# Performance work log

Measured on AMD Instinct MI355X. Metric: run time of the kernel, lower is better.

The kernel has to match this reference:

```python
import jax, jax.numpy as jnp
import numpy as np


def setup_inputs() -> dict:
    key = jax.random.key(0)
    ks = jax.random.split(key, 8)
    B, N, H = 8, 64, 256
    nE, E = 256, 64
    HID, OUT = 512, 1
    s1 = 1.0 / np.sqrt(H + E)
    s2 = 1.0 / np.sqrt(HID)
    return {
        "h_all": jax.random.normal(ks[0], (B, N, H), dtype=jnp.float32),
        "e_feat": jax.random.normal(ks[1], (nE, E), dtype=jnp.float32),
        "W1": jax.random.normal(ks[2], (H + E, HID), dtype=jnp.float32) * s1,
        "b1": jnp.zeros((HID,), dtype=jnp.float32),
        "W2": jax.random.normal(ks[3], (HID, HID), dtype=jnp.float32) * s2,
        "b2": jnp.zeros((HID,), dtype=jnp.float32),
        "W3": jax.random.normal(ks[4], (HID, OUT), dtype=jnp.float32) * s2,
        "b3": jnp.zeros((OUT,), dtype=jnp.float32),
    }


def reference(h_all, e_feat, W1, b1, W2, b2, W3, b3):
    # Math == MLP(cat([expand(h), expand(e)], -1)) but computed via split
    # weights: cat([h,e]) @ W1 == h @ W1[:H] + e @ W1[H:], avoiding the
    # materialized [B,N,nE,H+E] concat tensor.
    H = h_all.shape[-1]
    Wh, We = W1[:H], W1[H:]
    h_part = jnp.einsum("bnh,hk->bnk", h_all, Wh)        # [B,N,HID]
    e_part = jnp.einsum("ed,dk->ek", e_feat, We)          # [nE,HID]
    x = h_part[:, :, None, :] + e_part[None, None, :, :] + b1  # [B,N,nE,HID]
    x = jax.nn.relu(x)
    x = jax.nn.relu(jnp.einsum("bnek,kj->bnej", x, W2) + b2)
    return jnp.einsum("bnek,ko->bneo", x, W3) + b3        # [B,N,nE,OUT]
```

## Files before the change

kernel.cpp:

```cpp
#include <hip/hip_runtime.h>
#include <hip/hip_bf16.h>


typedef __attribute__((ext_vector_type(8))) short bf16x8;
typedef __attribute__((ext_vector_type(4))) float f32x4;

static __device__ __forceinline__ ushort2 pk_bf16(float a, float b) {
  union { __hip_bfloat162 h; ushort2 u; } c;
  c.h = __float22bfloat162_rn(make_float2(a, b));
  return c.u;
}
static __device__ __forceinline__ float bf2f(unsigned short u) {
  union { unsigned int i; float f; } c;
  c.i = ((unsigned int)u) << 16;
  return c.f;
}

__global__ __launch_bounds__(256) void k_prep(
    const float* __restrict__ h_all, const float* __restrict__ e_feat,
    const float* __restrict__ W1, const float* __restrict__ b1,
    const float* __restrict__ W2,
    unsigned short* __restrict__ hpb, unsigned short* __restrict__ epb,
    unsigned short* __restrict__ w2f) {
  __shared__ float sm[64 * 68];
  const int t = threadIdx.x;
  const int b = blockIdx.x;

  if (b < 256) {
    const int r0 = b * 2;
    float (*hs)[256] = (float(*)[256])sm;
    hs[0][t] = h_all[(size_t)r0 * 256 + t];
    hs[1][t] = h_all[(size_t)(r0 + 1) * 256 + t];
    __syncthreads();
    float2 a0 = make_float2(0.f, 0.f), a1 = make_float2(0.f, 0.f);
    #pragma unroll 2
    for (int k = 0; k < 256; k += 4) {
      float2 w0 = *(const float2*)(W1 + (size_t)k * 512 + 2 * t);
      float2 w1 = *(const float2*)(W1 + (size_t)(k + 1) * 512 + 2 * t);
      float2 w2v = *(const float2*)(W1 + (size_t)(k + 2) * 512 + 2 * t);
      float2 w3v = *(const float2*)(W1 + (size_t)(k + 3) * 512 + 2 * t);
      float h00 = hs[0][k], h01 = hs[0][k + 1], h02 = hs[0][k + 2], h03 = hs[0][k + 3];
      float h10 = hs[1][k], h11 = hs[1][k + 1], h12 = hs[1][k + 2], h13 = hs[1][k + 3];
      a0.x = fmaf(h00, w0.x, a0.x); a0.y = fmaf(h00, w0.y, a0.y);
      a1.x = fmaf(h10, w0.x, a1.x); a1.y = fmaf(h10, w0.y, a1.y);
      a0.x = fmaf(h01, w1.x, a0.x); a0.y = fmaf(h01, w1.y, a0.y);
      a1.x = fmaf(h11, w1.x, a1.x); a1.y = fmaf(h11, w1.y, a1.y);
      a0.x = fmaf(h02, w2v.x, a0.x); a0.y = fmaf(h02, w2v.y, a0.y);
      a1.x = fmaf(h12, w2v.x, a1.x); a1.y = fmaf(h12, w2v.y, a1.y);
      a0.x = fmaf(h03, w3v.x, a0.x); a0.y = fmaf(h03, w3v.y, a0.y);
      a1.x = fmaf(h13, w3v.x, a1.x); a1.y = fmaf(h13, w3v.y, a1.y);
    }
    float2 bv = *(const float2*)(b1 + 2 * t);
    *(ushort2*)(hpb + (size_t)r0 * 512 + 2 * t) = pk_bf16(a0.x + bv.x, a0.y + bv.y);
    *(ushort2*)(hpb + (size_t)(r0 + 1) * 512 + 2 * t) = pk_bf16(a1.x + bv.x, a1.y + bv.y);
  } else if (b < 288) {
    const int r0 = (b - 256) * 8;
    sm[t] = e_feat[(size_t)r0 * 64 + t];
    sm[256 + t] = e_feat[(size_t)r0 * 64 + 256 + t];
    __syncthreads();
    float2 acc[8];
    #pragma unroll
    for (int i = 0; i < 8; ++i) acc[i] = make_float2(0.f, 0.f);
    for (int k = 0; k < 64; ++k) {
      float2 wv = *(const float2*)(W1 + (size_t)(256 + k) * 512 + 2 * t);
      #pragma unroll
      for (int i = 0; i < 8; ++i) {
        acc[i].x = fmaf(sm[i * 64 + k], wv.x, acc[i].x);
        acc[i].y = fmaf(sm[i * 64 + k], wv.y, acc[i].y);
      }
    }
    #pragma unroll
    for (int i = 0; i < 8; ++i)
      *(ushort2*)(epb + (size_t)(r0 + i) * 512 + 2 * t) = pk_bf16(acc[i].x, acc[i].y);
  } else {
    const int bb = b - 288;
    const int k0 = (bb >> 3) * 64;
    const int c0 = (bb & 7) * 64;
    #pragma unroll
    for (int rr = 0; rr < 4; ++rr) {
      const int row = rr * 16 + (t >> 4);
      float4 v = *(const float4*)(W2 + (size_t)(k0 + row) * 512 + c0 + (t & 15) * 4);
      *(float4*)(&sm[row * 68 + (t & 15) * 4]) = v;
    }
    __syncthreads();
    #pragma unroll
    for (int s2 = 0; s2 < 2; ++s2) {
      const int s = t * 2 + s2;
      const int rec = s >> 6, l = s & 63;
      const int jg = (c0 >> 4) + (rec & 3);
      const int ksg = (k0 >> 5) + (rec >> 2);
      const int cl = (rec & 3) * 16 + (l & 15);
      const int kl = (rec >> 2) * 32 + (l >> 4) * 8;
      union { ushort2 o[4]; uint4 v; } u;
      #pragma unroll
      for (int uu = 0; uu < 4; ++uu)
        u.o[uu] = pk_bf16(sm[(kl + 2 * uu) * 68 + cl], sm[(kl + 2 * uu + 1) * 68 + cl]);
      *(uint4*)(w2f + ((size_t)(jg * 16 + ksg) * 64 + l) * 8) = u.v;
    }
  }
}

__global__ __launch_bounds__(256, 2) void k_main(
    const unsigned short* __restrict__ hpb, const unsigned short* __restrict__ epb,
    const unsigned short* __restrict__ w2f, const float* __restrict__ b2,
    const float* __restrict__ W3, const float* __restrict__ b3,
    float* __restrict__ out) {
  __shared__ unsigned short x1s[64 * 512];

  const int t = threadIdx.x;
  const int lane = t & 63;
  const int w = t >> 6;
  const int l15 = lane & 15, l4 = lane >> 4;
  const int bn = blockIdx.x >> 2;
  const int e0 = (blockIdx.x & 3) << 6;
  const int off = (blockIdx.x * 11) & 15;
  const unsigned short* hprow = hpb + (size_t)bn * 512;

  const unsigned short* wrec = w2f + (size_t)w * 65536 + (size_t)lane * 8;
  bf16x8 bb[2][8];
  #pragma unroll
  for (int j = 0; j < 8; ++j) {
    bb[0][j] = *(const bf16x8*)(wrec + j * 8192 + (size_t)off * 512);
    bb[1][j] = *(const bf16x8*)(wrec + j * 8192 + (size_t)((off + 1) & 15) * 512);
  }

  {
    const int kk = t & 63;
    const int rbase = t >> 6;
    union { uint4 v; unsigned short s[8]; } hv, ev, ov;
    hv.v = *(const uint4*)(hprow + kk * 8);
    float hf[8];
    #pragma unroll
    for (int u = 0; u < 8; ++u) hf[u] = bf2f(hv.s[u]);
    #pragma unroll 2
    for (int rr = 0; rr < 16; ++rr) {
      const int r = rr * 4 + rbase;
      ev.v = *(const uint4*)(epb + (size_t)(e0 + r) * 512 + kk * 8);
      #pragma unroll
      for (int u = 0; u < 4; ++u) {
        ushort2 p = pk_bf16(fmaxf(bf2f(ev.s[2 * u]) + hf[2 * u], 0.f),
                            fmaxf(bf2f(ev.s[2 * u + 1]) + hf[2 * u + 1], 0.f));
        ov.s[2 * u] = p.x;
        ov.s[2 * u + 1] = p.y;
      }
      *(uint4*)(&x1s[r * 512 + (kk ^ (r & 7)) * 8]) = ov.v;
    }
  }
  __syncthreads();

  f32x4 acc[4][8] = {};
  #pragma unroll 4
  for (int ks = 0; ks < 16; ++ks) {
    const int cur = ks & 1;
    const int kr = (ks + off) & 15;
    const int kr2 = (ks + 2 + off) & 15;
    bf16x8 a[4];
    #pragma unroll
    for (int i = 0; i < 4; ++i) {
      const int r = i * 16 + l15;
      a[i] = *(const bf16x8*)(&x1s[r * 512 + (((kr * 4 + l4) ^ (l15 & 7)) * 8)]);
    }
    #pragma unroll
    for (int i = 0; i < 4; ++i)
      #pragma unroll
      for (int j = 0; j < 8; ++j)
        acc[i][j] = __builtin_amdgcn_mfma_f32_16x16x32_bf16(a[i], bb[cur][j], acc[i][j], 0, 0, 0);
    #pragma unroll
    for (int j = 0; j < 8; ++j)
      bb[cur][j] = *(const bf16x8*)(wrec + j * 8192 + (size_t)kr2 * 512);
  }

  float part[16];
  #pragma unroll
  for (int u = 0; u < 16; ++u) part[u] = 0.f;
  #pragma unroll
  for (int j = 0; j < 8; ++j) {
    const int n = w * 128 + j * 16 + l15;
    const float b2v = b2[n], w3v = W3[n];
    #pragma unroll
    for (int i = 0; i < 4; ++i)
      #pragma unroll
      for (int r = 0; r < 4; ++r)
        part[i * 4 + r] = fmaf(fmaxf(acc[i][j][r] + b2v, 0.f), w3v, part[i * 4 + r]);
  }
  #pragma unroll
  for (int u = 0; u < 16; ++u) {
    float v = part[u];
    v += __shfl_xor(v, 1);
    v += __shfl_xor(v, 2);
    v += __shfl_xor(v, 4);
    v += __shfl_xor(v, 8);
    part[u] = v;
  }
  __syncthreads();
  float* osum = (float*)x1s;
  if (l15 == 0) {
    #pragma unroll
    for (int i = 0; i < 4; ++i)
      #pragma unroll
      for (int r = 0; r < 4; ++r)
        osum[w * 64 + i * 16 + l4 * 4 + r] = part[i * 4 + r];
  }
  __syncthreads();
  if (t < 64) {
    float s = b3[0] + osum[t] + osum[64 + t] + osum[128 + t] + osum[192 + t];
    out[(size_t)bn * 256 + e0 + t] = s;
  }
}

extern "C" void kernel_launch(void* const* d_in, const int* in_sizes, int n_in,
                              void* d_out, int out_size, void* d_ws, size_t ws_size,
                              hipStream_t stream) {
  const float* h_all  = (const float*)d_in[0];
  const float* e_feat = (const float*)d_in[1];
  const float* W1     = (const float*)d_in[2];
  const float* b1     = (const float*)d_in[3];
  const float* W2     = (const float*)d_in[4];
  const float* b2     = (const float*)d_in[5];
  const float* W3     = (const float*)d_in[6];
  const float* b3     = (const float*)d_in[7];
  float* out = (float*)d_out;

  unsigned short* hpb = (unsigned short*)d_ws;
  unsigned short* epb = hpb + 512 * 512;
  unsigned short* w2f = epb + 256 * 512;

  hipLaunchKernelGGL(k_prep, dim3(352), dim3(256), 0, stream,
                     h_all, e_feat, W1, b1, W2, hpb, epb, w2f);
  hipLaunchKernelGGL(k_main, dim3(2048), dim3(256), 0, stream,
                     hpb, epb, w2f, b2, W3, b3, out);
}
```

Before: 145.1 us.

## Persistent k_main with register-resident W2 slice and double-buffered x1 tiles

k_main becomes a persistent kernel: 512 blocks of 512 threads, each keeping its half of the W2 columns (a 32-column strip per wave) resident in registers for the whole run. It loops over 8 tiles, building the next relu(h+e) tile in a second LDS buffer while MFMAs consume the current one, so W2 is no longer reloaded from global memory for every tile. Splitting the hidden dimension in two adds a partial-sum workspace and a third combine kernel that adds the halves and b3. This costs higher register pressure (32 bf16x8 fragments per lane), more LDS, and an extra launch.

```diff
diff --git a/kernel.cpp b/kernel.cpp
--- a/kernel.cpp
+++ b/kernel.cpp
@@ -100,112 +100,161 @@
   }
 }
 
-__global__ __launch_bounds__(256, 2) void k_main(
+__global__ __launch_bounds__(512, 2) void k_main(
     const unsigned short* __restrict__ hpb, const unsigned short* __restrict__ epb,
     const unsigned short* __restrict__ w2f, const float* __restrict__ b2,
-    const float* __restrict__ W3, const float* __restrict__ b3,
-    float* __restrict__ out) {
-  __shared__ unsigned short x1s[64 * 512];
+    const float* __restrict__ W3, float* __restrict__ pws) {
+  __shared__ unsigned short x1s[2][64 * 512];
+  __shared__ float osum[2][8][64];
 
   const int t = threadIdx.x;
   const int lane = t & 63;
   const int w = t >> 6;
   const int l15 = lane & 15, l4 = lane >> 4;
-  const int bn = blockIdx.x >> 2;
-  const int e0 = (blockIdx.x & 3) << 6;
-  const int off = (blockIdx.x * 11) & 15;
-  const unsigned short* hprow = hpb + (size_t)bn * 512;
-
-  const unsigned short* wrec = w2f + (size_t)w * 65536 + (size_t)lane * 8;
-  bf16x8 bb[2][8];
+  const int p = lane & 7;
+  const int cg = blockIdx.x & 1;
+  const int stream = blockIdx.x >> 1;
+
+  bf16x8 bfr[2][16];
+  {
+    const unsigned short* wb = w2f + ((size_t)(cg * 16 + w * 2) * 16 * 64 + lane) * 8;
+    #pragma unroll
+    for (int j = 0; j < 2; ++j)
+      #pragma unroll
+      for (int ks = 0; ks < 16; ++ks)
+        bfr[j][ks] = *(const bf16x8*)(wb + (size_t)(j * 16 + ks) * 512);
+  }
+  float b2v[2], w3v[2];
   #pragma unroll
-  for (int j = 0; j < 8; ++j) {
-    bb[0][j] = *(const bf16x8*)(wrec + j * 8192 + (size_t)off * 512);
-    bb[1][j] = *(const bf16x8*)(wrec + j * 8192 + (size_t)((off + 1) & 15) * 512);
-  }
+  for (int j = 0; j < 2; ++j) {
+    const int n = cg * 256 + w * 32 + j * 16 + l15;
+    b2v[j] = b2[n];
+    w3v[j] = W3[n];
+  }
+
+  const int kk = t & 63;
+  const int rb = t >> 6;
+  unsigned short* sb[2];
+  sb[0] = &x1s[0][rb * 512 + ((kk ^ rb) * 8)];
+  sb[1] = &x1s[1][rb * 512 + ((kk ^ rb) * 8)];
+  const int c0 = l4 ^ p;
+  const unsigned short* ab[2][2];
+  ab[0][0] = &x1s[0][l15 * 512 + c0 * 8];
+  ab[0][1] = &x1s[0][l15 * 512 + (c0 ^ 4) * 8];
+  ab[1][0] = &x1s[1][l15 * 512 + c0 * 8];
+  ab[1][1] = &x1s[1][l15 * 512 + (c0 ^ 4) * 8];
 
   {
-    const int kk = t & 63;
-    const int rbase = t >> 6;
-    union { uint4 v; unsigned short s[8]; } hv, ev, ov;
-    hv.v = *(const uint4*)(hprow + kk * 8);
+    const int tt0 = stream * 8;
+    const unsigned short* hpr = hpb + (size_t)(tt0 >> 2) * 512 + kk * 8;
+    const unsigned short* epr = epb + ((size_t)(((tt0 & 3) << 6) + rb)) * 512 + kk * 8;
+    union { uint4 v; unsigned short s[8]; } hv, ev, nx, ov;
+    hv.v = *(const uint4*)hpr;
+    ev.v = *(const uint4*)epr;
     float hf[8];
     #pragma unroll
     for (int u = 0; u < 8; ++u) hf[u] = bf2f(hv.s[u]);
-    #pragma unroll 2
-    for (int rr = 0; rr < 16; ++rr) {
-      const int r = rr * 4 + rbase;
-      ev.v = *(const uint4*)(epb + (size_t)(e0 + r) * 512 + kk * 8);
+    #pragma unroll
+    for (int s = 0; s < 8; ++s) {
+      if (s < 7) nx.v = *(const uint4*)(epr + (size_t)(s + 1) * 4096);
       #pragma unroll
       for (int u = 0; u < 4; ++u) {
-        ushort2 p = pk_bf16(fmaxf(bf2f(ev.s[2 * u]) + hf[2 * u], 0.f),
-                            fmaxf(bf2f(ev.s[2 * u + 1]) + hf[2 * u + 1], 0.f));
-        ov.s[2 * u] = p.x;
-        ov.s[2 * u + 1] = p.y;
-      }
-      *(uint4*)(&x1s[r * 512 + (kk ^ (r & 7)) * 8]) = ov.v;
+        ushort2 pk = pk_bf16(fmaxf(bf2f(ev.s[2 * u]) + hf[2 * u], 0.f),
+                             fmaxf(bf2f(ev.s[2 * u + 1]) + hf[2 * u + 1], 0.f));
+        ov.s[2 * u] = pk.x;
+        ov.s[2 * u + 1] = pk.y;
+      }
+      *(uint4*)(sb[0] + (size_t)s * 4096) = ov.v;
+      ev = nx;
     }
   }
   __syncthreads();
 
-  f32x4 acc[4][8] = {};
-  #pragma unroll 4
-  for (int ks = 0; ks < 16; ++ks) {
-    const int cur = ks & 1;
-    const int kr = (ks + off) & 15;
-    const int kr2 = (ks + 2 + off) & 15;
-    bf16x8 a[4];
-    #pragma unroll
-    for (int i = 0; i < 4; ++i) {
-      const int r = i * 16 + l15;
-      a[i] = *(const bf16x8*)(&x1s[r * 512 + (((kr * 4 + l4) ^ (l15 & 7)) * 8)]);
-    }
-    #pragma unroll
-    for (int i = 0; i < 4; ++i)
-      #pragma unroll
-      for (int j = 0; j < 8; ++j)
-        acc[i][j] = __builtin_amdgcn_mfma_f32_16x16x32_bf16(a[i], bb[cur][j], acc[i][j], 0, 0, 0);
-    #pragma unroll
-    for (int j = 0; j < 8; ++j)
-      bb[cur][j] = *(const bf16x8*)(wrec + j * 8192 + (size_t)kr2 * 512);
-  }
-
-  float part[16];
-  #pragma unroll
-  for (int u = 0; u < 16; ++u) part[u] = 0.f;
-  #pragma unroll
-  for (int j = 0; j < 8; ++j) {
-    const int n = w * 128 + j * 16 + l15;
-    const float b2v = b2[n], w3v = W3[n];
-    #pragma unroll
-    for (int i = 0; i < 4; ++i)
-      #pragma unroll
-      for (int r = 0; r < 4; ++r)
-        part[i * 4 + r] = fmaf(fmaxf(acc[i][j][r] + b2v, 0.f), w3v, part[i * 4 + r]);
-  }
-  #pragma unroll
-  for (int u = 0; u < 16; ++u) {
-    float v = part[u];
-    v += __shfl_xor(v, 1);
-    v += __shfl_xor(v, 2);
-    v += __shfl_xor(v, 4);
-    v += __shfl_xor(v, 8);
-    part[u] = v;
-  }
-  __syncthreads();
-  float* osum = (float*)x1s;
-  if (l15 == 0) {
-    #pragma unroll
-    for (int i = 0; i < 4; ++i)
-      #pragma unroll
-      for (int r = 0; r < 4; ++r)
-        osum[w * 64 + i * 16 + l4 * 4 + r] = part[i * 4 + r];
-  }
-  __syncthreads();
-  if (t < 64) {
-    float s = b3[0] + osum[t] + osum[64 + t] + osum[128 + t] + osum[192 + t];
-    out[(size_t)bn * 256 + e0 + t] = s;
-  }
+  #pragma unroll 1
+  for (int st = 0; st < 8; ++st) {
+    const int q = st & 1, qn = q ^ 1;
+    const int stn = (st < 7) ? st + 1 : st;
+    const int ttn = stream * 8 + stn;
+    const unsigned short* hpr = hpb + (size_t)(ttn >> 2) * 512 + kk * 8;
+    const unsigned short* epr = epb + ((size_t)(((ttn & 3) << 6) + rb)) * 512 + kk * 8;
+    union { uint4 v; unsigned short s[8]; } hv, evc, evn, ov;
+    hv.v = *(const uint4*)hpr;
+    evc.v = *(const uint4*)epr;
+    float hf[8];
+    #pragma unroll
+    for (int u = 0; u < 8; ++u) hf[u] = bf2f(hv.s[u]);
+
+    f32x4 acc[4][2] = {};
+    #pragma unroll
+    for (int ks = 0; ks < 16; ++ks) {
+      const int m = ks >> 1;
+      bf16x8 a[4];
+      #pragma unroll
+      for (int i = 0; i < 4; ++i)
+        a[i] = *(const bf16x8*)(ab[q][ks & 1] + i * 8192 + m * 64);
+      #pragma unroll
+      for (int i = 0; i < 4; ++i) {
+        acc[i][0] = __builtin_amdgcn_mfma_f32_16x16x32_bf16(a[i], bfr[0][ks], acc[i][0], 0, 0, 0);
+        acc[i][1] = __builtin_amdgcn_mfma_f32_16x16x32_bf16(a[i], bfr[1][ks], acc[i][1], 0, 0, 0);
+      }
+      if ((ks & 1) == 0) {
+        const int s1 = (ks >> 1) + 1;
+        if (s1 < 8) evn.v = *(const uint4*)(epr + (size_t)s1 * 4096);
+      } else {
+        const int s = ks >> 1;
+        #pragma unroll
+        for (int u = 0; u < 4; ++u) {
+          ushort2 pk = pk_bf16(fmaxf(bf2f(evc.s[2 * u]) + hf[2 * u], 0.f),
+                               fmaxf(bf2f(evc.s[2 * u + 1]) + hf[2 * u + 1], 0.f));
+          ov.s[2 * u] = pk.x;
+          ov.s[2 * u + 1] = pk.y;
+        }
+        *(uint4*)(sb[qn] + (size_t)s * 4096) = ov.v;
+        evc = evn;
+      }
+    }
+
+    float part[16];
+    #pragma unroll
+    for (int u = 0; u < 16; ++u) part[u] = 0.f;
+    #pragma unroll
+    for (int j = 0; j < 2; ++j)
+      #pragma unroll
+      for (int i = 0; i < 4; ++i)
+        #pragma unroll
+        for (int r = 0; r < 4; ++r)
+          part[i * 4 + r] = fmaf(fmaxf(acc[i][j][r] + b2v[j], 0.f), w3v[j], part[i * 4 + r]);
+    #pragma unroll
+    for (int u = 0; u < 16; ++u) {
+      float v = part[u];
+      v += __shfl_xor(v, 1);
+      v += __shfl_xor(v, 2);
+      v += __shfl_xor(v, 4);
+      v += __shfl_xor(v, 8);
+      part[u] = v;
+    }
+    if (l15 == 0) {
+      #pragma unroll
+      for (int i = 0; i < 4; ++i)
+        #pragma unroll
+        for (int r = 0; r < 4; ++r)
+          osum[q][w][i * 16 + l4 * 4 + r] = part[i * 4 + r];
+    }
+    __syncthreads();
+    if (t < 64) {
+      float s = 0.f;
+      #pragma unroll
+      for (int ww = 0; ww < 8; ++ww) s += osum[q][ww][t];
+      pws[(size_t)cg * 131072 + (size_t)(stream * 8 + st) * 64 + t] = s;
+    }
+  }
+}
+
+__global__ __launch_bounds__(256) void k_comb(const float* __restrict__ pws,
+                                              const float* __restrict__ b3,
+                                              float* __restrict__ out) {
+  const int i = blockIdx.x * 256 + threadIdx.x;
+  out[i] = pws[i] + pws[131072 + i] + b3[0];
 }
 
 extern "C" void kernel_launch(void* const* d_in, const int* in_sizes, int n_in,
@@ -224,9 +273,12 @@
   unsigned short* hpb = (unsigned short*)d_ws;
   unsigned short* epb = hpb + 512 * 512;
   unsigned short* w2f = epb + 256 * 512;
+  float* pws = (float*)(w2f + 512 * 512);
 
   hipLaunchKernelGGL(k_prep, dim3(352), dim3(256), 0, stream,
                      h_all, e_feat, W1, b1, W2, hpb, epb, w2f);
-  hipLaunchKernelGGL(k_main, dim3(2048), dim3(256), 0, stream,
-                     hpb, epb, w2f, b2, W3, b3, out);
-}
+  hipLaunchKernelGGL(k_main, dim3(512), dim3(512), 0, stream,
+                     hpb, epb, w2f, b2, W3, pws);
+  hipLaunchKernelGGL(k_comb, dim3(512), dim3(256), 0, stream,
+                     pws, b3, out);
+}
```

Result: slower. 188.4 us (+29.9%).

## Restructure main GEMM into 128-row blocks with double-buffered K-chunk staging in LDS

Applied to the files above, without the earlier changes.

The main kernel now gives each block 128 edge rows (512 threads, 8 waves in a 2x4 row/column layout) in place of 64 rows with 4 waves. W2 is no longer streamed by every wave straight from global memory into registers. W2 K-slices and the fused relu(h+e) activations are staged per 32-wide K chunk into double-buffered shared memory, and the next chunk's global loads overlap the current MFMAs. This halves the W2 global traffic per output row and cuts LDS to small chunk buffers. In exchange it adds a block-wide barrier on every K step.

```diff
diff --git a/kernel.cpp b/kernel.cpp
--- a/kernel.cpp
+++ b/kernel.cpp
@@ -100,74 +100,104 @@
   }
 }
 
-__global__ __launch_bounds__(256, 2) void k_main(
+__global__ __launch_bounds__(512, 2) void k_main(
     const unsigned short* __restrict__ hpb, const unsigned short* __restrict__ epb,
     const unsigned short* __restrict__ w2f, const float* __restrict__ b2,
     const float* __restrict__ W3, const float* __restrict__ b3,
     float* __restrict__ out) {
-  __shared__ unsigned short x1s[64 * 512];
+  __shared__ unsigned short x1s[2][128 * 32];
+  __shared__ unsigned short bs[2][32 * 512];
+  __shared__ float osum[2][4][64];
 
   const int t = threadIdx.x;
   const int lane = t & 63;
   const int w = t >> 6;
+  const int rq = w >> 2;
+  const int cq = w & 3;
   const int l15 = lane & 15, l4 = lane >> 4;
-  const int bn = blockIdx.x >> 2;
-  const int e0 = (blockIdx.x & 3) << 6;
-  const int off = (blockIdx.x * 11) & 15;
-  const unsigned short* hprow = hpb + (size_t)bn * 512;
-
-  const unsigned short* wrec = w2f + (size_t)w * 65536 + (size_t)lane * 8;
-  bf16x8 bb[2][8];
-  #pragma unroll
-  for (int j = 0; j < 8; ++j) {
-    bb[0][j] = *(const bf16x8*)(wrec + j * 8192 + (size_t)off * 512);
-    bb[1][j] = *(const bf16x8*)(wrec + j * 8192 + (size_t)((off + 1) & 15) * 512);
-  }
+  const int bn = blockIdx.x >> 1;
+  const int e0 = (blockIdx.x & 1) << 7;
+
+  const int sr = t >> 2;
+  const int sc = t & 3;
+  const unsigned short* eprow = epb + (size_t)(e0 + sr) * 512 + sc * 8;
+  const unsigned short* hprow = hpb + (size_t)bn * 512 + sc * 8;
+  unsigned short* x1w[2];
+  x1w[0] = &x1s[0][sr * 32 + ((sc ^ (sr & 3)) * 8)];
+  x1w[1] = &x1s[1][sr * 32 + ((sc ^ (sr & 3)) * 8)];
+  const int arow = rq * 64 + l15;
+  const int achk = (l4 ^ (l15 & 3)) * 8;
 
   {
-    const int kk = t & 63;
-    const int rbase = t >> 6;
+    uint4 hv4 = *(const uint4*)(hprow);
+    uint4 ev4 = *(const uint4*)(eprow);
     union { uint4 v; unsigned short s[8]; } hv, ev, ov;
-    hv.v = *(const uint4*)(hprow + kk * 8);
-    float hf[8];
-    #pragma unroll
-    for (int u = 0; u < 8; ++u) hf[u] = bf2f(hv.s[u]);
-    #pragma unroll 2
-    for (int rr = 0; rr < 16; ++rr) {
-      const int r = rr * 4 + rbase;
-      ev.v = *(const uint4*)(epb + (size_t)(e0 + r) * 512 + kk * 8);
+    hv.v = hv4; ev.v = ev4;
+    #pragma unroll
+    for (int u = 0; u < 4; ++u) {
+      ushort2 p = pk_bf16(fmaxf(bf2f(ev.s[2 * u]) + bf2f(hv.s[2 * u]), 0.f),
+                          fmaxf(bf2f(ev.s[2 * u + 1]) + bf2f(hv.s[2 * u + 1]), 0.f));
+      ov.s[2 * u] = p.x;
+      ov.s[2 * u + 1] = p.y;
+    }
+    *(uint4*)x1w[0] = ov.v;
+    #pragma unroll
+    for (int i = 0; i < 4; ++i) {
+      const int s = i * 512 + t;
+      const int rec = s >> 6, ln = s & 63;
+      uint4 bv = *(const uint4*)(w2f + ((size_t)(rec * 16 + 0) * 64 + ln) * 8);
+      *(uint4*)(&bs[0][(size_t)(rec * 64 + ln) * 8]) = bv;
+    }
+  }
+  __syncthreads();
+
+  f32x4 acc[4][8] = {};
+  #pragma unroll 1
+  for (int kc = 0; kc < 16; ++kc) {
+    const int q = kc & 1, qn = q ^ 1;
+    const int kn = (kc < 15) ? kc + 1 : kc;
+    uint4 hv4 = *(const uint4*)(hprow + kn * 32);
+    uint4 ev4 = *(const uint4*)(eprow + kn * 32);
+    uint4 bv4[4];
+    #pragma unroll
+    for (int i = 0; i < 4; ++i) {
+      const int s = i * 512 + t;
+      const int rec = s >> 6, ln = s & 63;
+      bv4[i] = *(const uint4*)(w2f + ((size_t)(rec * 16 + kn) * 64 + ln) * 8);
+    }
+    {
+      bf16x8 a[4], b[8];
+      #pragma unroll
+      for (int i = 0; i < 4; ++i)
+        a[i] = *(const bf16x8*)(&x1s[q][(arow + i * 16) * 32 + achk]);
+      #pragma unroll
+      for (int j = 0; j < 8; ++j)
+        b[j] = *(const bf16x8*)(&bs[q][(size_t)((cq * 8 + j) * 64 + lane) * 8]);
+      #pragma unroll
+      for (int i = 0; i < 4; ++i)
+        #pragma unroll
+        for (int j = 0; j < 8; ++j)
+          acc[i][j] = __builtin_amdgcn_mfma_f32_16x16x32_bf16(a[i], b[j], acc[i][j], 0, 0, 0);
+    }
+    if (kc < 15) {
+      union { uint4 v; unsigned short s[8]; } hv, ev, ov;
+      hv.v = hv4; ev.v = ev4;
       #pragma unroll
       for (int u = 0; u < 4; ++u) {
-        ushort2 p = pk_bf16(fmaxf(bf2f(ev.s[2 * u]) + hf[2 * u], 0.f),
-                            fmaxf(bf2f(ev.s[2 * u + 1]) + hf[2 * u + 1], 0.f));
+        ushort2 p = pk_bf16(fmaxf(bf2f(ev.s[2 * u]) + bf2f(hv.s[2 * u]), 0.f),
+                            fmaxf(bf2f(ev.s[2 * u + 1]) + bf2f(hv.s[2 * u + 1]), 0.f));
         ov.s[2 * u] = p.x;
         ov.s[2 * u + 1] = p.y;
       }
-      *(uint4*)(&x1s[r * 512 + (kk ^ (r & 7)) * 8]) = ov.v;
-    }
-  }
-  __syncthreads();
-
-  f32x4 acc[4][8] = {};
-  #pragma unroll 4
-  for (int ks = 0; ks < 16; ++ks) {
-    const int cur = ks & 1;
-    const int kr = (ks + off) & 15;
-    const int kr2 = (ks + 2 + off) & 15;
-    bf16x8 a[4];
-    #pragma unroll
-    for (int i = 0; i < 4; ++i) {
-      const int r = i * 16 + l15;
-      a[i] = *(const bf16x8*)(&x1s[r * 512 + (((kr * 4 + l4) ^ (l15 & 7)) * 8)]);
-    }
-    #pragma unroll
-    for (int i = 0; i < 4; ++i)
-      #pragma unroll
-      for (int j = 0; j < 8; ++j)
-        acc[i][j] = __builtin_amdgcn_mfma_f32_16x16x32_bf16(a[i], bb[cur][j], acc[i][j], 0, 0, 0);
-    #pragma unroll
-    for (int j = 0; j < 8; ++j)
-      bb[cur][j] = *(const bf16x8*)(wrec + j * 8192 + (size_t)kr2 * 512);
+      *(uint4*)x1w[qn] = ov.v;
+      #pragma unroll
+      for (int i = 0; i < 4; ++i) {
+        const int s = i * 512 + t;
+        const int rec = s >> 6, ln = s & 63;
+        *(uint4*)(&bs[qn][(size_t)(rec * 64 + ln) * 8]) = bv4[i];
+      }
+    }
+    __syncthreads();
   }
 
   float part[16];
@@ -175,7 +205,7 @@
   for (int u = 0; u < 16; ++u) part[u] = 0.f;
   #pragma unroll
   for (int j = 0; j < 8; ++j) {
-    const int n = w * 128 + j * 16 + l15;
+    const int n = cq * 128 + j * 16 + l15;
     const float b2v = b2[n], w3v = W3[n];
     #pragma unroll
     for (int i = 0; i < 4; ++i)
@@ -192,18 +222,17 @@
     v += __shfl_xor(v, 8);
     part[u] = v;
   }
+  if (l15 == 0) {
+    #pragma unroll
+    for (int i = 0; i < 4; ++i)
+      #pragma unroll
+      for (int r = 0; r < 4; ++r)
+        osum[rq][cq][i * 16 + l4 * 4 + r] = part[i * 4 + r];
+  }
   __syncthreads();
-  float* osum = (float*)x1s;
-  if (l15 == 0) {
-    #pragma unroll
-    for (int i = 0; i < 4; ++i)
-      #pragma unroll
-      for (int r = 0; r < 4; ++r)
-        osum[w * 64 + i * 16 + l4 * 4 + r] = part[i * 4 + r];
-  }
-  __syncthreads();
-  if (t < 64) {
-    float s = b3[0] + osum[t] + osum[64 + t] + osum[128 + t] + osum[192 + t];
+  if (t < 128) {
+    const int r2 = t >> 6, ri = t & 63;
+    float s = b3[0] + osum[r2][0][ri] + osum[r2][1][ri] + osum[r2][2][ri] + osum[r2][3][ri];
     out[(size_t)bn * 256 + e0 + t] = s;
   }
 }
@@ -227,6 +256,6 @@
 
   hipLaunchKernelGGL(k_prep, dim3(352), dim3(256), 0, stream,
                      h_all, e_feat, W1, b1, W2, hpb, epb, w2f);
-  hipLaunchKernelGGL(k_main, dim3(2048), dim3(256), 0, stream,
+  hipLaunchKernelGGL(k_main, dim3(1024), dim3(512), 0, stream,
                      hpb, epb, w2f, b2, W3, b3, out);
 }
```

Measured after the change: 159.7 us. +10.1%, slower.

## Switch main GEMM to 32x32x16 MFMA with 8 waves per block

Applied to the files above, without the earlier changes.

Replaces the 16x16x32 bf16 MFMA tiling with 32x32x16 MFMA. The block grows to 512 threads (8 waves), each wave owning a 64-column slice of W2 output, and the W2 fragment layout in the prep kernel changes to match. The x1 tile in LDS is stored pre-swizzled in MFMA operand order, so A loads become lane-contiguous, and the reduction epilogue is adapted to 8 waves. The aim is higher MFMA throughput and occupancy with fewer registers per wave. In exchange, each wave now streams its W2 slice from global memory with little reuse, and the per-block offset rotation is dropped.

```diff
diff --git a/kernel.cpp b/kernel.cpp
--- a/kernel.cpp
+++ b/kernel.cpp
@@ -3,7 +3,7 @@
 
 
 typedef __attribute__((ext_vector_type(8))) short bf16x8;
-typedef __attribute__((ext_vector_type(4))) float f32x4;
+typedef __attribute__((ext_vector_type(16))) float f32x16;
 
 static __device__ __forceinline__ ushort2 pk_bf16(float a, float b) {
   union { __hip_bfloat162 h; ushort2 u; } c;
@@ -73,9 +73,9 @@
     for (int i = 0; i < 8; ++i)
       *(ushort2*)(epb + (size_t)(r0 + i) * 512 + 2 * t) = pk_bf16(acc[i].x, acc[i].y);
   } else {
-    const int bb = b - 288;
-    const int k0 = (bb >> 3) * 64;
-    const int c0 = (bb & 7) * 64;
+    const int bb2 = b - 288;
+    const int k0 = (bb2 >> 3) * 64;
+    const int c0 = (bb2 & 7) * 64;
     #pragma unroll
     for (int rr = 0; rr < 4; ++rr) {
       const int row = rr * 16 + (t >> 4);
@@ -87,123 +87,121 @@
     for (int s2 = 0; s2 < 2; ++s2) {
       const int s = t * 2 + s2;
       const int rec = s >> 6, l = s & 63;
-      const int jg = (c0 >> 4) + (rec & 3);
-      const int ksg = (k0 >> 5) + (rec >> 2);
-      const int cl = (rec & 3) * 16 + (l & 15);
-      const int kl = (rec >> 2) * 32 + (l >> 4) * 8;
+      const int jg = (c0 >> 5) + (rec & 1);
+      const int ks = (k0 >> 4) + (rec >> 1);
+      const int cl = (rec & 1) * 32 + (l & 31);
+      const int kl = (rec >> 1) * 16 + (l >> 5) * 8;
       union { ushort2 o[4]; uint4 v; } u;
       #pragma unroll
       for (int uu = 0; uu < 4; ++uu)
         u.o[uu] = pk_bf16(sm[(kl + 2 * uu) * 68 + cl], sm[(kl + 2 * uu + 1) * 68 + cl]);
-      *(uint4*)(w2f + ((size_t)(jg * 16 + ksg) * 64 + l) * 8) = u.v;
-    }
-  }
-}
-
-__global__ __launch_bounds__(256, 2) void k_main(
+      *(uint4*)(w2f + ((size_t)(jg * 32 + ks) * 64 + l) * 8) = u.v;
+    }
+  }
+}
+
+__global__ __launch_bounds__(512, 4) void k_main(
     const unsigned short* __restrict__ hpb, const unsigned short* __restrict__ epb,
     const unsigned short* __restrict__ w2f, const float* __restrict__ b2,
     const float* __restrict__ W3, const float* __restrict__ b3,
     float* __restrict__ out) {
   __shared__ unsigned short x1s[64 * 512];
+  __shared__ float osum[8][64];
 
   const int t = threadIdx.x;
   const int lane = t & 63;
   const int w = t >> 6;
-  const int l15 = lane & 15, l4 = lane >> 4;
+  const int l31 = lane & 31;
+  const int half = lane >> 5;
   const int bn = blockIdx.x >> 2;
   const int e0 = (blockIdx.x & 3) << 6;
-  const int off = (blockIdx.x * 11) & 15;
-  const unsigned short* hprow = hpb + (size_t)bn * 512;
-
-  const unsigned short* wrec = w2f + (size_t)w * 65536 + (size_t)lane * 8;
-  bf16x8 bb[2][8];
-  #pragma unroll
-  for (int j = 0; j < 8; ++j) {
-    bb[0][j] = *(const bf16x8*)(wrec + j * 8192 + (size_t)off * 512);
-    bb[1][j] = *(const bf16x8*)(wrec + j * 8192 + (size_t)((off + 1) & 15) * 512);
-  }
+
+  const unsigned short* wrec0 = w2f + ((size_t)(w * 2 + 0) * 32 * 64 + lane) * 8;
+  const unsigned short* wrec1 = w2f + ((size_t)(w * 2 + 1) * 32 * 64 + lane) * 8;
+  bf16x8 bb[2][2];
+  bb[0][0] = *(const bf16x8*)(wrec0);
+  bb[0][1] = *(const bf16x8*)(wrec1);
+  bb[1][0] = *(const bf16x8*)(wrec0 + 512);
+  bb[1][1] = *(const bf16x8*)(wrec1 + 512);
 
   {
-    const int kk = t & 63;
-    const int rbase = t >> 6;
-    union { uint4 v; unsigned short s[8]; } hv, ev, ov;
-    hv.v = *(const uint4*)(hprow + kk * 8);
-    float hf[8];
-    #pragma unroll
-    for (int u = 0; u < 8; ++u) hf[u] = bf2f(hv.s[u]);
-    #pragma unroll 2
-    for (int rr = 0; rr < 16; ++rr) {
-      const int r = rr * 4 + rbase;
-      ev.v = *(const uint4*)(epb + (size_t)(e0 + r) * 512 + kk * 8);
+    const int r = t >> 3;
+    const int c8 = t & 7;
+    const unsigned short* hrow = hpb + (size_t)bn * 512 + c8 * 8;
+    const unsigned short* erow = epb + (size_t)(e0 + r) * 512 + c8 * 8;
+    const int slot = (r & 31) + ((c8 & 1) << 5);
+    const int rec0 = (r >> 5) * 32 + (c8 >> 1);
+    #pragma unroll
+    for (int i = 0; i < 8; ++i) {
+      union { uint4 v; unsigned short s[8]; } hv, ev, ov;
+      hv.v = *(const uint4*)(hrow + i * 64);
+      ev.v = *(const uint4*)(erow + i * 64);
       #pragma unroll
       for (int u = 0; u < 4; ++u) {
-        ushort2 p = pk_bf16(fmaxf(bf2f(ev.s[2 * u]) + hf[2 * u], 0.f),
-                            fmaxf(bf2f(ev.s[2 * u + 1]) + hf[2 * u + 1], 0.f));
+        ushort2 p = pk_bf16(fmaxf(bf2f(ev.s[2 * u]) + bf2f(hv.s[2 * u]), 0.f),
+                            fmaxf(bf2f(ev.s[2 * u + 1]) + bf2f(hv.s[2 * u + 1]), 0.f));
         ov.s[2 * u] = p.x;
         ov.s[2 * u + 1] = p.y;
       }
-      *(uint4*)(&x1s[r * 512 + (kk ^ (r & 7)) * 8]) = ov.v;
+      *(uint4*)(&x1s[((rec0 + i * 4) * 64 + slot) * 8]) = ov.v;
     }
   }
   __syncthreads();
 
-  f32x4 acc[4][8] = {};
-  #pragma unroll 4
-  for (int ks = 0; ks < 16; ++ks) {
+  f32x16 acc[2][2] = {};
+  const unsigned short* abase = x1s + (size_t)lane * 8;
+  #pragma unroll 8
+  for (int ks = 0; ks < 32; ++ks) {
     const int cur = ks & 1;
-    const int kr = (ks + off) & 15;
-    const int kr2 = (ks + 2 + off) & 15;
-    bf16x8 a[4];
-    #pragma unroll
-    for (int i = 0; i < 4; ++i) {
-      const int r = i * 16 + l15;
-      a[i] = *(const bf16x8*)(&x1s[r * 512 + (((kr * 4 + l4) ^ (l15 & 7)) * 8)]);
-    }
-    #pragma unroll
-    for (int i = 0; i < 4; ++i)
-      #pragma unroll
-      for (int j = 0; j < 8; ++j)
-        acc[i][j] = __builtin_amdgcn_mfma_f32_16x16x32_bf16(a[i], bb[cur][j], acc[i][j], 0, 0, 0);
-    #pragma unroll
-    for (int j = 0; j < 8; ++j)
-      bb[cur][j] = *(const bf16x8*)(wrec + j * 8192 + (size_t)kr2 * 512);
-  }
-
-  float part[16];
+    const int kn = (ks + 2) & 31;
+    bf16x8 a0 = *(const bf16x8*)(abase + (size_t)(0 * 32 + ks) * 512);
+    bf16x8 a1 = *(const bf16x8*)(abase + (size_t)(1 * 32 + ks) * 512);
+    acc[0][0] = __builtin_amdgcn_mfma_f32_32x32x16_bf16(a0, bb[cur][0], acc[0][0], 0, 0, 0);
+    acc[0][1] = __builtin_amdgcn_mfma_f32_32x32x16_bf16(a0, bb[cur][1], acc[0][1], 0, 0, 0);
+    acc[1][0] = __builtin_amdgcn_mfma_f32_32x32x16_bf16(a1, bb[cur][0], acc[1][0], 0, 0, 0);
+    acc[1][1] = __builtin_amdgcn_mfma_f32_32x32x16_bf16(a1, bb[cur][1], acc[1][1], 0, 0, 0);
+    bb[cur][0] = *(const bf16x8*)(wrec0 + (size_t)kn * 512);
+    bb[cur][1] = *(const bf16x8*)(wrec1 + (size_t)kn * 512);
+  }
+
+  float b2v[2], w3v[2];
   #pragma unroll
-  for (int u = 0; u < 16; ++u) part[u] = 0.f;
+  for (int ct = 0; ct < 2; ++ct) {
+    const int n = w * 64 + ct * 32 + l31;
+    b2v[ct] = b2[n];
+    w3v[ct] = W3[n];
+  }
   #pragma unroll
-  for (int j = 0; j < 8; ++j) {
-    const int n = w * 128 + j * 16 + l15;
-    const float b2v = b2[n], w3v = W3[n];
-    #pragma unroll
-    for (int i = 0; i < 4; ++i)
-      #pragma unroll
-      for (int r = 0; r < 4; ++r)
-        part[i * 4 + r] = fmaf(fmaxf(acc[i][j][r] + b2v, 0.f), w3v, part[i * 4 + r]);
-  }
-  #pragma unroll
-  for (int u = 0; u < 16; ++u) {
-    float v = part[u];
-    v += __shfl_xor(v, 1);
-    v += __shfl_xor(v, 2);
-    v += __shfl_xor(v, 4);
-    v += __shfl_xor(v, 8);
-    part[u] = v;
-  }
-  __syncthreads();
-  float* osum = (float*)x1s;
-  if (l15 == 0) {
-    #pragma unroll
-    for (int i = 0; i < 4; ++i)
-      #pragma unroll
-      for (int r = 0; r < 4; ++r)
-        osum[w * 64 + i * 16 + l4 * 4 + r] = part[i * 4 + r];
+  for (int rt = 0; rt < 2; ++rt) {
+    float part[16];
+    #pragma unroll
+    for (int g = 0; g < 16; ++g) {
+      part[g] = fmaf(fmaxf(acc[rt][0][g] + b2v[0], 0.f), w3v[0], 0.f);
+      part[g] = fmaf(fmaxf(acc[rt][1][g] + b2v[1], 0.f), w3v[1], part[g]);
+    }
+    #pragma unroll
+    for (int g = 0; g < 16; ++g) {
+      float v = part[g];
+      v += __shfl_xor(v, 1);
+      v += __shfl_xor(v, 2);
+      v += __shfl_xor(v, 4);
+      v += __shfl_xor(v, 8);
+      v += __shfl_xor(v, 16);
+      part[g] = v;
+    }
+    if (l31 == 0) {
+      #pragma unroll
+      for (int g = 0; g < 16; ++g) {
+        const int row = rt * 32 + (g & 3) + 8 * (g >> 2) + 4 * half;
+        osum[w][row] = part[g];
+      }
+    }
   }
   __syncthreads();
   if (t < 64) {
-    float s = b3[0] + osum[t] + osum[64 + t] + osum[128 + t] + osum[192 + t];
+    float s = b3[0];
+    #pragma unroll
+    for (int ww = 0; ww < 8; ++ww) s += osum[ww][t];
     out[(size_t)bn * 256 + e0 + t] = s;
   }
 }
@@ -227,6 +225,6 @@
 
   hipLaunchKernelGGL(k_prep, dim3(352), dim3(256), 0, stream,
                      h_all, e_feat, W1, b1, W2, hpb, epb, w2f);
-  hipLaunchKernelGGL(k_main, dim3(2048), dim3(256), 0, stream,
+  hipLaunchKernelGGL(k_main, dim3(2048), dim3(512), 0, stream,
                      hpb, epb, w2f, b2, W3, b3, out);
 }
```

Measured after the change: 162.7 us. +12.2%, slower.
